# Kernel optimization log

Hardware: AMD Instinct MI355X
Metric: run time of the kernel (lower is better)

## Reference

```python
import jax, jax.numpy as jnp
import numpy as np

NB_BINS = 10
N = 33554432  # 2**25 elements


def setup_inputs() -> dict:
    key = jax.random.key(0)
    k1, k2 = jax.random.split(key)
    logits = jax.random.normal(k1, (N,), dtype=jnp.float32)
    labels = jax.random.randint(k2, (N,), 0, 2, dtype=jnp.int32)
    return {"logits": logits, "labels": labels}


def reference(logits, labels):
    # confidences in (0,1); bins are (l, u] over linspace(0,1,nb+1),
    # so bin index = ceil(conf * nb) - 1, clipped to [0, nb-1].
    conf = jax.nn.sigmoid(logits)
    idx = jnp.clip(jnp.ceil(conf * NB_BINS).astype(jnp.int32) - 1, 0, NB_BINS - 1)

    counts = jax.ops.segment_sum(jnp.ones_like(conf), idx, num_segments=NB_BINS)
    sum_conf = jax.ops.segment_sum(conf, idx, num_segments=NB_BINS)
    sum_pos = jax.ops.segment_sum(labels.astype(conf.dtype), idx, num_segments=NB_BINS)

    denom = jnp.maximum(counts, 1.0)
    nonempty = counts > 0
    positives_per_bin = jnp.where(nonempty, sum_pos / denom, 0.0)
    confidence_per_bin = jnp.where(nonempty, sum_conf / denom, 0.0)
    return jnp.stack([positives_per_bin, confidence_per_bin])  # [2, nb_bins]
```

## Files before the change

### kernel.cpp

```cpp
#include <hip/hip_runtime.h>

typedef unsigned int u32;
typedef unsigned long long u64;

#define NB 10
#define BLOCKS 1024
#define TPB 256
#define ITERS 32
#define DEPTH 4
#define WAVE_F4 (ITERS * 64)

__global__ void rd_zero_ws(u32* __restrict__ ws) {
    if (threadIdx.x < 320) ws[threadIdx.x] = 0u;
}

__device__ __forceinline__ void rd_acc(float x, int lab,
                                       u64& c64, u64& p64, u64& flo, u64& fhi) {
    float e = __expf(-x);
    float conf = __builtin_amdgcn_rcpf(1.0f + e);
    float t10 = __builtin_fmaf(conf, 10.0f, -1e-6f);
    int b = min(9, (int)t10);
    float frac = t10 - (float)b;
    u32 ffx = (u32)__builtin_fmaf(frac, 127.0f, 0.5f);

    u32 sh6 = (u32)(b * 6);
    c64 += 1ull << sh6;
    p64 += ((u64)(u32)lab) << sh6;

    bool lo = b < 5;
    u32 sh12 = (u32)(b * 12);
    u32 shf = lo ? sh12 : (sh12 - 60u);
    u64 v = ((u64)ffx) << shf;
    flo += lo ? v : 0ull;
    fhi += lo ? 0ull : v;
}

__device__ __forceinline__ void rd_acc4(const float4& x, const int4& y,
                                        u64& c64, u64& p64, u64& flo, u64& fhi) {
    rd_acc(x.x, y.x, c64, p64, flo, fhi);
    rd_acc(x.y, y.y, c64, p64, flo, fhi);
    rd_acc(x.z, y.z, c64, p64, flo, fhi);
    rd_acc(x.w, y.w, c64, p64, flo, fhi);
}

__global__ __launch_bounds__(TPB, 4) void rd_hist(const float* __restrict__ logits,
                                                  const int* __restrict__ labels,
                                                  u32* __restrict__ ws,
                                                  long long n) {
    u32 cp[NB], cf[NB];
    #pragma unroll
    for (int b = 0; b < NB; ++b) { cp[b] = 0u; cf[b] = 0u; }

    const float4* l4 = (const float4*)logits;
    const int4*   i4 = (const int4*)labels;
    int lane = threadIdx.x & 63;
    int wave = threadIdx.x >> 6;
    long long nf4 = n >> 2;
    long long seg = (long long)blockIdx.x * (4 * WAVE_F4);

    u64 c64 = 0, p64 = 0, flo = 0, fhi = 0;

    #define UNPACK() do {                                                   \
        _Pragma("unroll")                                                   \
        for (int b = 0; b < NB; ++b) {                                      \
            u32 cnt = (u32)(c64 >> (6 * b)) & 63u;                          \
            u32 pos = (u32)(p64 >> (6 * b)) & 63u;                          \
            cp[b] += cnt | (pos << 16);                                     \
            cf[b] += (b < 5) ? ((u32)(flo >> (12 * b)) & 4095u)             \
                             : ((u32)(fhi >> (12 * (b - 5))) & 4095u);      \
        }                                                                   \
        c64 = 0; p64 = 0; flo = 0; fhi = 0;                                 \
    } while (0)

    if (seg + 4 * WAVE_F4 <= nf4) {
        long long gb = seg + (long long)wave * WAVE_F4;
        const float4* gl = l4 + gb + lane;
        const int4*   gi = i4 + gb + lane;

        float4 px0 = gl[0 * 64], px1 = gl[1 * 64], px2 = gl[2 * 64], px3 = gl[3 * 64];
        int4   py0 = gi[0 * 64], py1 = gi[1 * 64], py2 = gi[2 * 64], py3 = gi[3 * 64];

        #pragma unroll
        for (int t = 0; t < ITERS; ++t) {
            const int s = t & 3;
            float4 x; int4 y;
            if      (s == 0) { x = px0; y = py0; }
            else if (s == 1) { x = px1; y = py1; }
            else if (s == 2) { x = px2; y = py2; }
            else             { x = px3; y = py3; }
            if (t + DEPTH < ITERS) {
                if      (s == 0) { px0 = gl[(t + DEPTH) * 64]; py0 = gi[(t + DEPTH) * 64]; }
                else if (s == 1) { px1 = gl[(t + DEPTH) * 64]; py1 = gi[(t + DEPTH) * 64]; }
                else if (s == 2) { px2 = gl[(t + DEPTH) * 64]; py2 = gi[(t + DEPTH) * 64]; }
                else             { px3 = gl[(t + DEPTH) * 64]; py3 = gi[(t + DEPTH) * 64]; }
            }
            rd_acc4(x, y, c64, p64, flo, fhi);
            if ((t & 7) == 7) UNPACK();
        }
    }

    long long done_f4 = ((long long)gridDim.x < nf4 / (4 * WAVE_F4)
                             ? (long long)gridDim.x
                             : nf4 / (4 * WAVE_F4)) * (4 * WAVE_F4);
    long long tail = done_f4 * 4;
    if (tail < n) {
        long long tid    = (long long)blockIdx.x * blockDim.x + threadIdx.x;
        long long stride = (long long)gridDim.x * blockDim.x;
        for (long long i = tail + tid; i < n; i += stride) {
            float e = __expf(-logits[i]);
            float conf = __builtin_amdgcn_rcpf(1.0f + e);
            float t10 = __builtin_fmaf(conf, 10.0f, -1e-6f);
            int b = min(9, (int)t10);
            float frac = t10 - (float)b;
            u32 ffx = (u32)__builtin_fmaf(frac, 127.0f, 0.5f);
            atomicAdd((u64*)&ws[32 * b], (u64)ffx);
            atomicAdd(&ws[32 * b + 2], 1u);
            atomicAdd(&ws[32 * b + 3], (u32)labels[i]);
        }
    }
    #undef UNPACK

    __shared__ u32 s_cp[4][NB];
    __shared__ u32 s_cf[4][NB];
    #pragma unroll
    for (int b = 0; b < NB; ++b) {
        u32 c = cp[b];
        u32 f = cf[b];
        #pragma unroll
        for (int off = 32; off; off >>= 1) {
            c += __shfl_down(c, off, 64);
            f += __shfl_down(f, off, 64);
        }
        if (lane == 0) { s_cp[wave][b] = c; s_cf[wave][b] = f; }
    }
    __syncthreads();

    if (threadIdx.x < NB) {
        int b = threadIdx.x;
        u32 c = s_cp[0][b] + s_cp[1][b] + s_cp[2][b] + s_cp[3][b];
        u64 f = (u64)s_cf[0][b] + s_cf[1][b] + s_cf[2][b] + s_cf[3][b];
        atomicAdd((u64*)&ws[32 * b], f);
        atomicAdd(&ws[32 * b + 2], c & 0xFFFFu);
        atomicAdd(&ws[32 * b + 3], c >> 16);
    }
}

__global__ void rd_finalize(const u32* __restrict__ ws, float* __restrict__ out) {
    int b = threadIdx.x;
    if (b < NB) {
        u64 f   = *(const u64*)&ws[32 * b];
        u32 cnt = ws[32 * b + 2];
        u32 pos = ws[32 * b + 3];
        double sumconf = ((double)b * (double)cnt + (double)f * (1.0 / 127.0)) * 0.1;
        float denom = fmaxf((float)cnt, 1.0f);
        bool ne = cnt > 0u;
        out[b]      = ne ? ((float)pos / denom) : 0.0f;
        out[NB + b] = ne ? (float)(sumconf / (double)denom) : 0.0f;
    }
}

extern "C" void kernel_launch(void* const* d_in, const int* in_sizes, int n_in,
                              void* d_out, int out_size, void* d_ws, size_t ws_size,
                              hipStream_t stream) {
    const float* logits = (const float*)d_in[0];
    const int*   labels = (const int*)d_in[1];
    float* out = (float*)d_out;
    u32*   ws  = (u32*)d_ws;
    long long n = (long long)in_sizes[0];

    rd_zero_ws<<<1, 512, 0, stream>>>(ws);
    rd_hist<<<BLOCKS, TPB, 0, stream>>>(logits, labels, ws, n);
    rd_finalize<<<1, 64, 0, stream>>>(ws, out);
}
```

Baseline: 296.1 us.

## Use block-strided coalesced layout with more blocks and higher occupancy

```diff
diff --git a/kernel.cpp b/kernel.cpp
--- a/kernel.cpp
+++ b/kernel.cpp
@@ -4,11 +4,9 @@
 typedef unsigned long long u64;
 
 #define NB 10
-#define BLOCKS 1024
+#define BLOCKS 2048
 #define TPB 256
-#define ITERS 32
-#define DEPTH 4
-#define WAVE_F4 (ITERS * 64)
+#define F4_PER_BLOCK 4096
 
 __global__ void rd_zero_ws(u32* __restrict__ ws) {
     if (threadIdx.x < 320) ws[threadIdx.x] = 0u;
@@ -43,20 +41,13 @@
     rd_acc(x.w, y.w, c64, p64, flo, fhi);
 }
 
-__global__ __launch_bounds__(TPB, 4) void rd_hist(const float* __restrict__ logits,
+__global__ __launch_bounds__(TPB, 8) void rd_hist(const float* __restrict__ logits,
                                                   const int* __restrict__ labels,
                                                   u32* __restrict__ ws,
                                                   long long n) {
     u32 cp[NB], cf[NB];
     #pragma unroll
     for (int b = 0; b < NB; ++b) { cp[b] = 0u; cf[b] = 0u; }
-
-    const float4* l4 = (const float4*)logits;
-    const int4*   i4 = (const int4*)labels;
-    int lane = threadIdx.x & 63;
-    int wave = threadIdx.x >> 6;
-    long long nf4 = n >> 2;
-    long long seg = (long long)blockIdx.x * (4 * WAVE_F4);
 
     u64 c64 = 0, p64 = 0, flo = 0, fhi = 0;
 
@@ -72,36 +63,33 @@
         c64 = 0; p64 = 0; flo = 0; fhi = 0;                                 \
     } while (0)
 
-    if (seg + 4 * WAVE_F4 <= nf4) {
-        long long gb = seg + (long long)wave * WAVE_F4;
-        const float4* gl = l4 + gb + lane;
-        const int4*   gi = i4 + gb + lane;
+    long long nf4 = n >> 2;
+    long long segll = (long long)blockIdx.x * F4_PER_BLOCK;
 
-        float4 px0 = gl[0 * 64], px1 = gl[1 * 64], px2 = gl[2 * 64], px3 = gl[3 * 64];
-        int4   py0 = gi[0 * 64], py1 = gi[1 * 64], py2 = gi[2 * 64], py3 = gi[3 * 64];
+    if (segll + F4_PER_BLOCK <= nf4) {
+        int seg = (int)segll + (int)threadIdx.x;
+        const float4* gl = (const float4*)logits + seg;
+        const int4*   gi = (const int4*)labels + seg;
 
         #pragma unroll
-        for (int t = 0; t < ITERS; ++t) {
-            const int s = t & 3;
-            float4 x; int4 y;
-            if      (s == 0) { x = px0; y = py0; }
-            else if (s == 1) { x = px1; y = py1; }
-            else if (s == 2) { x = px2; y = py2; }
-            else             { x = px3; y = py3; }
-            if (t + DEPTH < ITERS) {
-                if      (s == 0) { px0 = gl[(t + DEPTH) * 64]; py0 = gi[(t + DEPTH) * 64]; }
-                else if (s == 1) { px1 = gl[(t + DEPTH) * 64]; py1 = gi[(t + DEPTH) * 64]; }
-                else if (s == 2) { px2 = gl[(t + DEPTH) * 64]; py2 = gi[(t + DEPTH) * 64]; }
-                else             { px3 = gl[(t + DEPTH) * 64]; py3 = gi[(t + DEPTH) * 64]; }
+        for (int h = 0; h < 2; ++h) {
+            #pragma unroll
+            for (int g = 0; g < 4; ++g) {
+                const int k = (h * 8 + g * 2) * 256;
+                float4 x0 = gl[k];
+                int4   y0 = gi[k];
+                float4 x1 = gl[k + 256];
+                int4   y1 = gi[k + 256];
+                rd_acc4(x0, y0, c64, p64, flo, fhi);
+                rd_acc4(x1, y1, c64, p64, flo, fhi);
             }
-            rd_acc4(x, y, c64, p64, flo, fhi);
-            if ((t & 7) == 7) UNPACK();
+            UNPACK();
         }
     }
 
-    long long done_f4 = ((long long)gridDim.x < nf4 / (4 * WAVE_F4)
+    long long done_f4 = ((long long)gridDim.x < nf4 / F4_PER_BLOCK
                              ? (long long)gridDim.x
-                             : nf4 / (4 * WAVE_F4)) * (4 * WAVE_F4);
+                             : nf4 / F4_PER_BLOCK) * F4_PER_BLOCK;
     long long tail = done_f4 * 4;
     if (tail < n) {
         long long tid    = (long long)blockIdx.x * blockDim.x + threadIdx.x;
@@ -122,6 +110,8 @@
 
     __shared__ u32 s_cp[4][NB];
     __shared__ u32 s_cf[4][NB];
+    int lane = threadIdx.x & 63;
+    int wave = threadIdx.x >> 6;
     #pragma unroll
     for (int b = 0; b < NB; ++b) {
         u32 c = cp[b];
```

After: 321.2 us. +8.5%, slower.
